# Kernel optimization log

Hardware: AMD Instinct MI355X
Metric: run time of the kernel (lower is better)

The kernel has to match this reference:

```python
import jax, jax.numpy as jnp
import numpy as np


def _gen_grid(h, w, stride=1):
    """Normalized spherical sampling grid, shape (3*H', 3*W', 2) with (x, y) order,
    matching gen_grid_coordinates in the torch source (vectorized)."""
    pi = np.pi
    dphi = pi / h
    dth = 2 * pi / w
    t = np.tan(dth)
    p = np.tan(dphi)
    sp = p / np.cos(dth)
    # xys[kr, kc] = (x, y) tangent-plane offsets of the 3x3 kernel taps
    xys = np.array([[[-t, sp], [0.0, p], [t, sp]],
                    [[-t, 0.0], [1.0, 1.0], [t, 0.0]],
                    [[-t, -sp], [0.0, -p], [t, -sp]]], dtype=np.float64)
    X = xys[..., 0]
    Y = xys[..., 1]
    rho = np.sqrt(X ** 2 + Y ** 2)           # [3,3], nonzero everywhere
    v = np.arctan(rho)
    rr = np.arange(0, h, stride)
    cc = np.arange(0, w, stride)
    phi = -((rr + 0.5) / h * pi - pi / 2)    # [H']
    theta = (cc + 0.5) / w * 2 * pi - pi     # [W']
    sphi = np.sin(phi)[:, None, None, None]  # [H',1,1,1]
    cphi = np.cos(phi)[:, None, None, None]
    arg = np.cos(v) * sphi + Y * np.sin(v) * cphi / rho  # [H',1,3,3]
    new_phi = np.arcsin(np.clip(arg, -1.0, 1.0))
    new_theta = theta[None, :, None, None] + np.arctan(
        X * np.sin(v) / (rho * cphi * np.cos(v) - Y * sphi * np.sin(v)))  # [H',W',3,3]
    new_r = np.broadcast_to((-new_phi + pi / 2) * h / pi - 0.5, new_theta.shape).copy()
    new_c = (new_theta + pi) * w / (2 * pi) - 0.5
    new_c = (new_c + w) % w
    # center tap samples the pixel itself
    new_r[:, :, 1, 1] = rr[:, None]
    new_c[:, :, 1, 1] = cc[None, :]
    gx = new_c * 2 / w - 1
    gy = new_r * 2 / h - 1
    grid = np.stack([gx, gy], axis=-1)                     # [H',W',3,3,2]
    Hp, Wp = len(rr), len(cc)
    grid = grid.transpose(0, 2, 1, 3, 4).reshape(Hp * 3, Wp * 3, 2)
    return grid.astype(np.float32)


def _grid_sample_bilinear_zeros(x, grid):
    """torch grid_sample(mode='bilinear', padding_mode='zeros', align_corners=False).
    x: [N,C,H,W]; grid: [Hg,Wg,2] (shared over batch). Returns [N,C,Hg,Wg]."""
    N, C, H, W = x.shape
    ix = ((grid[..., 0] + 1) * W - 1) * 0.5
    iy = ((grid[..., 1] + 1) * H - 1) * 0.5
    x0 = jnp.floor(ix)
    y0 = jnp.floor(iy)
    x1 = x0 + 1
    y1 = y0 + 1
    wx1 = ix - x0
    wx0 = 1.0 - wx1
    wy1 = iy - y0
    wy0 = 1.0 - wy1

    def gather(yy, xx):
        valid = ((xx >= 0) & (xx <= W - 1) & (yy >= 0) & (yy <= H - 1)).astype(x.dtype)
        xi = jnp.clip(xx, 0, W - 1).astype(jnp.int32)
        yi = jnp.clip(yy, 0, H - 1).astype(jnp.int32)
        return x[:, :, yi, xi], valid  # [N,C,Hg,Wg], [Hg,Wg]

    v00, m00 = gather(y0, x0)
    v01, m01 = gather(y0, x1)
    v10, m10 = gather(y1, x0)
    v11, m11 = gather(y1, x1)
    return (v00 * (wy0 * wx0 * m00) + v01 * (wy0 * wx1 * m01)
            + v10 * (wy1 * wx0 * m10) + v11 * (wy1 * wx1 * m11))


def setup_inputs() -> dict:
    key = jax.random.key(0)
    k1, k2, k3 = jax.random.split(key, 3)
    N, Cin, H, W = 4, 64, 128, 256
    Cout = 128
    x = jax.random.normal(k1, (N, Cin, H, W), dtype=jnp.float32)
    fan_in = Cin * 9
    bound = 1.0 / np.sqrt(fan_in)
    weight = jax.random.uniform(k2, (Cout, Cin, 3, 3), dtype=jnp.float32,
                                minval=-bound, maxval=bound)
    bias = jnp.zeros((Cout,), dtype=jnp.float32)
    return {"x": x, "weight": weight, "bias": bias}


def reference(x, weight, bias):
    H, W = int(x.shape[2]), int(x.shape[3])
    grid = jnp.asarray(_gen_grid(H, W, 1))              # [3H, 3W, 2]
    s = _grid_sample_bilinear_zeros(x, grid)            # [N, Cin, 3H, 3W]
    y = jax.lax.conv_general_dilated(
        s, weight, window_strides=(3, 3), padding='VALID',
        dimension_numbers=('NCHW', 'OIHW', 'NCHW'))     # [N, Cout, H, W]
    return y + bias[None, :, None, None]
```

## Files before the change

kernel.cpp:

```cpp
#include <hip/hip_runtime.h>
#include <math.h>

typedef __attribute__((ext_vector_type(8))) _Float16 half8;
typedef __attribute__((ext_vector_type(4))) _Float16 half4;
typedef __attribute__((ext_vector_type(2))) _Float16 half2;
typedef __attribute__((ext_vector_type(4))) float floatx4;
typedef __attribute__((ext_vector_type(4))) unsigned int uintx4;

#define NB    4
#define CIN   64
#define COUT  128
#define IMH   128
#define IMW   256
#define KTOT  576
#define NPIX  (IMH * IMW)
#define PXT   128
#define NDPB  (PXT * 9)
#define ROWS  4
#define KCH   96
#define DSTR  520
#define XT_OFF 262144
#define XT_BYTES ((size_t)NB * 8 * IMH * IMW * 16)

__device__ __forceinline__ unsigned pkrtz2(float a, float b) {
  unsigned r;
  asm("v_cvt_pkrtz_f16_f32 %0, %1, %2" : "=v"(r) : "v"(a), "v"(b));
  return r;
}
__device__ __forceinline__ half4 bcl(unsigned u) {
  half2 h; __builtin_memcpy(&h, &u, 4);
  return __builtin_shufflevector(h, h, 0, 0, 0, 0);
}
__device__ __forceinline__ half4 bch(unsigned u) {
  half2 h; __builtin_memcpy(&h, &u, 4);
  return __builtin_shufflevector(h, h, 1, 1, 1, 1);
}
__device__ __forceinline__ half8 bcl8(unsigned u) {
  half2 h; __builtin_memcpy(&h, &u, 4);
  return __builtin_shufflevector(h, h, 0, 0, 0, 0, 0, 0, 0, 0);
}
__device__ __forceinline__ half8 bch8(unsigned u) {
  half2 h; __builtin_memcpy(&h, &u, 4);
  return __builtin_shufflevector(h, h, 1, 1, 1, 1, 1, 1, 1, 1);
}
__device__ __forceinline__ void gload_lds16(const void* g, void* l) {
  __builtin_amdgcn_global_load_lds(
      (const __attribute__((address_space(1))) unsigned int*)g,
      (__attribute__((address_space(3))) unsigned int*)l, 16, 0, 0);
}

__global__ __launch_bounds__(256) void prep_w_kernel(const float* __restrict__ w,
                                                     unsigned short* __restrict__ wbf) {
  int idx = blockIdx.x * 256 + threadIdx.x;
  if (idx >= COUT * 8 * KCH) return;
  int co = idx / (8 * KCH);
  int K2 = idx - co * (8 * KCH);
  int cb = K2 / KCH, kk = K2 - cb * KCH;
  unsigned short v = 0;
  if (kk < 72) {
    int t = kk >> 3, chl = kk & 7;
    int ci = cb * 8 + chl;
    _Float16 h = (_Float16)w[co * KTOT + ci * 9 + t];
    __builtin_memcpy(&v, &h, 2);
  }
  wbf[(K2 >> 3) * (COUT * 8) + co * 8 + (K2 & 7)] = v;
}

__global__ __launch_bounds__(256) void prep_x_kernel(const float* __restrict__ x,
                                                     unsigned short* __restrict__ xt) {
  int idx = blockIdx.x * 256 + threadIdx.x;
  int c   = idx & 255;
  int rr  = (idx >> 8) & 127;
  int ncb = idx >> 15;
  int n = ncb >> 3, cb = ncb & 7;
  const float* src = x + (size_t)(n * CIN + cb * 8) * NPIX + rr * IMW + c;
  unsigned o4[4];
  #pragma unroll
  for (int j = 0; j < 4; j++)
    o4[j] = pkrtz2(src[(size_t)(2 * j) * NPIX], src[(size_t)(2 * j + 1) * NPIX]);
  *(uintx4*)(xt + (size_t)idx * 8) = *(uintx4*)o4;
}

__global__ __launch_bounds__(512, 4) void sphconv_fast(
    const unsigned short* __restrict__ xt, const unsigned short* __restrict__ wbf,
    const float* __restrict__ bias, float* __restrict__ out) {
  __shared__ __align__(16) unsigned int stg[2][ROWS * IMW * 4];
  __shared__ __align__(16) unsigned int descL[12 * DSTR];
  __shared__ double tapA[9];
  __shared__ float  tapWy[9][2];
  __shared__ int    tapRo[9][2];

  const int tid  = threadIdx.x;
  const int lane = tid & 63;
  const int wv   = tid >> 6;
  const int lin = blockIdx.x + 2 * blockIdx.y;
  const int sw  = (lin & 7) * 32 + (lin >> 3);
  const int ct  = sw >> 7;
  const int r   = sw & 127;
  const int n   = blockIdx.z;
  const int c0  = ct * PXT;
  const int co_base = (wv & 1) * 64;
  const int px_base = (wv >> 1) * 32;
  const int rlo  = min(max(r - 2, 0), IMH - ROWS);
  const int q    = lane >> 4;
  const int p    = lane & 15;

  {
    const char* gs = (const char*)xt
        + ((size_t)((n * 8 + 0) * IMH + rlo) * IMW) * 16 + wv * 1024 + lane * 16;
    char* lb = (char*)&stg[0][0] + wv * 1024;
    gload_lds16(gs, lb);
    gload_lds16(gs + 8192, lb + 8192);
  }

  {
    int myk = -1;
    if (lane == 0) myk = wv;
    if (wv == 0 && lane == 32) myk = 8;
    if (myk >= 0) {
      const double pi = 3.14159265358979323846;
      double dphi = pi / IMH;
      double dth  = 2.0 * pi / IMW;
      double t  = tan(dth);
      double pp = tan(dphi);
      double sp_ = pp / cos(dth);
      double phi  = -(((double)r + 0.5) / IMH * pi - pi * 0.5);
      double sphi = sin(phi), cphi = cos(phi);
      int i = myk / 3, j = myk % 3;
      double atv, new_r;
      if (myk == 4) {
        atv = 0.0; new_r = (double)r;
      } else {
        double X = (j == 0) ? -t : ((j == 2) ? t : 0.0);
        double Y = 0.0;
        if (i == 0)      Y = (j == 1) ?  pp :  sp_;
        else if (i == 2) Y = (j == 1) ? -pp : -sp_;
        double rho = sqrt(X * X + Y * Y);
        double v   = atan(rho);
        double sv = sin(v), cv = cos(v);
        double arg = cv * sphi + Y * sv * cphi / rho;
        arg = fmin(1.0, fmax(-1.0, arg));
        double new_phi = asin(arg);
        double denom = rho * cphi * cv - Y * sphi * sv;
        atv = atan(X * sv / denom);
        new_r = (-new_phi + pi * 0.5) * IMH / pi - 0.5;
      }
      float gy = (float)(new_r * 2.0 / IMH - 1.0);
      float iy = ((gy + 1.0f) * (float)IMH - 1.0f) * 0.5f;
      float fy = floorf(iy); int y0 = (int)fy;
      float wy1 = iy - fy, wy0 = 1.0f - wy1;
      int y1 = y0 + 1;
      bool vy0 = (y0 >= 0) & (y0 <= IMH - 1);
      bool vy1 = (y1 >= 0) & (y1 <= IMH - 1);
      int y0c = min(max(y0, 0), IMH - 1), y1c = min(max(y1, 0), IMH - 1);
      int rt = min(max(y0c - rlo, 0), ROWS - 1);
      int rb = min(max(y1c - rlo, 0), ROWS - 1);
      tapA[myk] = atv;
      tapWy[myk][0] = vy0 ? wy0 : 0.0f;
      tapWy[myk][1] = vy1 ? wy1 : 0.0f;
      tapRo[myk][0] = rt * (IMW * 4);
      tapRo[myk][1] = rb * (IMW * 4);
    }
  }
  __syncthreads();

  {
    const double pi = 3.14159265358979323846;
    #pragma unroll
    for (int dd = 0; dd < 3; dd++) {
      if (dd < 2 || tid < NDPB - 1024) {
        int d  = tid + dd * 512;
        int px = d & (PXT - 1), k = d >> 7;
        int c  = c0 + px;
        double nc;
        if (k == 4) {
          nc = (double)c;
        } else {
          double theta = ((double)c + 0.5) / IMW * (2.0 * pi) - pi;
          double new_theta = theta + tapA[k];
          nc = (new_theta + pi) * IMW / (2.0 * pi) - 0.5;
          nc = fmod(nc + (double)IMW, (double)IMW);
        }
        float gx = (float)(nc * 2.0 / IMW - 1.0);
        float ix = ((gx + 1.0f) * (float)IMW - 1.0f) * 0.5f;
        float fx = floorf(ix); int x0 = (int)fx;
        float wx1 = ix - fx, wx0 = 1.0f - wx1;
        int x1 = x0 + 1;
        int x0c = max(x0, 0);
        float w_lo = (x0 >= 0) ? wx0 : wx1;
        float w_hi = (x0 >= 0) ? ((x1 <= IMW - 1) ? wx1 : 0.0f) : 0.0f;
        float wy0m = tapWy[k][0], wy1m = tapWy[k][1];
        int dc = (x1 <= IMW - 1) ? 4 : 0;
        int offt = tapRo[k][0] + x0c * 4;
        int offb = tapRo[k][1] + x0c * 4;
        uintx4 rec;
        rec.x = (unsigned)(offt | (offb << 16));
        rec.y = pkrtz2(wy0m * w_lo, wy0m * w_hi);
        rec.z = pkrtz2(wy1m * w_lo, wy1m * w_hi);
        rec.w = (unsigned)dc;
        *(uintx4*)&descL[k * DSTR + px * 4] = rec;
      }
    }
  }
  if (tid < 3 * PXT) {
    uintx4 zr = {0u, 0u, 0u, 0u};
    *(uintx4*)&descL[(9 + (tid >> 7)) * DSTR + (tid & (PXT - 1)) * 4] = zr;
  }

  floatx4 acc[4][2];
  #pragma unroll
  for (int mt = 0; mt < 4; mt++)
    #pragma unroll
    for (int nt = 0; nt < 2; nt++)
      acc[mt][nt] = (floatx4){0.f, 0.f, 0.f, 0.f};

  __syncthreads();

  #pragma unroll 1
  for (int cb = 0; cb < 8; cb++) {
    if (cb < 7) {
      const char* gs = (const char*)xt
          + ((size_t)((n * 8 + cb + 1) * IMH + rlo) * IMW) * 16 + wv * 1024 + lane * 16;
      char* lb = (char*)&stg[(cb + 1) & 1][0] + wv * 1024;
      gload_lds16(gs, lb);
      gload_lds16(gs + 8192, lb + 8192);
    }
    const unsigned int* sb = &stg[cb & 1][0];
    #pragma unroll
    for (int nt = 0; nt < 2; nt++) {
      const int pxl = px_base + nt * 16 + p;
      #pragma unroll
      for (int ks = 0; ks < 3; ks++) {
        uintx4 rec = *(const uintx4*)&descL[(ks * 4 + q) * DSTR + pxl * 4];
        unsigned op = rec.x;
        int dc = (int)rec.w;
        const unsigned int* pt = sb + (op & 0xFFFFu);
        const unsigned int* pb = sb + (op >> 16);
        half8 t0 = *(const half8*)pt;
        half8 t1 = *(const half8*)(pt + dc);
        half8 b0 = *(const half8*)pb;
        half8 b1 = *(const half8*)(pb + dc);
        half8 W0 = bcl8(rec.y), W1 = bch8(rec.y);
        half8 W2 = bcl8(rec.z), W3 = bch8(rec.z);
        half8 b = t0 * W0 + t1 * W1 + b0 * W2 + b1 * W3;
        const unsigned short* arow =
            wbf + (size_t)((cb * 12 + ks * 4 + q) * COUT + co_base + p) * 8;
        __builtin_amdgcn_s_setprio(1);
        #pragma unroll
        for (int mt = 0; mt < 4; mt++) {
          half8 a = *(const half8*)(arow + mt * 16 * 8);
          acc[mt][nt] = __builtin_amdgcn_mfma_f32_16x16x32_f16(a, b, acc[mt][nt], 0, 0, 0);
        }
        __builtin_amdgcn_s_setprio(0);
      }
    }
    __syncthreads();
  }

  #pragma unroll
  for (int mt = 0; mt < 4; mt++)
    #pragma unroll
    for (int nt = 0; nt < 2; nt++)
      #pragma unroll
      for (int rg = 0; rg < 4; rg++) {
        const int co = co_base + mt * 16 + q * 4 + rg;
        const int cc = c0 + px_base + nt * 16 + p;
        out[(((size_t)n * COUT + co) * IMH + r) * IMW + cc] = acc[mt][nt][rg] + bias[co];
      }
}

#define F_CSTW  6
#define F_NCOL  257
#define F_RSTW  (F_NCOL * F_CSTW)
__global__ __launch_bounds__(512, 4) void sphconv_fb(
    const float* __restrict__ x, const unsigned short* __restrict__ wbf,
    const float* __restrict__ bias, float* __restrict__ out) {
  __shared__ __align__(16) unsigned int stg[2][ROWS * F_RSTW];
  __shared__ __align__(16) unsigned int descL[12 * PXT * 4];
  __shared__ double tapA[9];
  __shared__ float  tapWy[9][2];
  __shared__ int    tapRo[9][2];

  const int tid  = threadIdx.x;
  const int lane = tid & 63;
  const int wv   = tid >> 6;
  const int lin = blockIdx.x + 2 * blockIdx.y;
  const int sw  = (lin & 7) * 32 + (lin >> 3);
  const int ct  = sw >> 7;
  const int r   = sw & 127;
  const int n   = blockIdx.z;
  const int c0  = ct * PXT;
  const int co_base = (wv & 1) * 64;
  const int px_base = (wv >> 1) * 32;
  const int rlo  = min(max(r - 2, 0), IMH - ROWS);
  const int q    = lane >> 4;
  const int p    = lane & 15;
  const int sp  = tid & 3;
  const int scg = (tid >> 2) & 63;
  const int srr = tid >> 8;

  const float* xn = x + (size_t)n * CIN * NPIX;

  floatx4 nx[4];
  #pragma unroll
  for (int c = 0; c < 2; c++)
    #pragma unroll
    for (int rw = 0; rw < 2; rw++)
      nx[c * 2 + rw] = *(const floatx4*)(xn + (size_t)(sp * 2 + c) * NPIX
                                         + (size_t)(rlo + srr * 2 + rw) * IMW + scg * 4);

  {
    int myk = -1;
    if (lane == 0) myk = wv;
    if (wv == 0 && lane == 32) myk = 8;
    if (myk >= 0) {
      const double pi = 3.14159265358979323846;
      double dphi = pi / IMH;
      double dth  = 2.0 * pi / IMW;
      double t  = tan(dth);
      double pp = tan(dphi);
      double sp_ = pp / cos(dth);
      double phi  = -(((double)r + 0.5) / IMH * pi - pi * 0.5);
      double sphi = sin(phi), cphi = cos(phi);
      int i = myk / 3, j = myk % 3;
      double atv, new_r;
      if (myk == 4) {
        atv = 0.0; new_r = (double)r;
      } else {
        double X = (j == 0) ? -t : ((j == 2) ? t : 0.0);
        double Y = 0.0;
        if (i == 0)      Y = (j == 1) ?  pp :  sp_;
        else if (i == 2) Y = (j == 1) ? -pp : -sp_;
        double rho = sqrt(X * X + Y * Y);
        double v   = atan(rho);
        double sv = sin(v), cv = cos(v);
        double arg = cv * sphi + Y * sv * cphi / rho;
        arg = fmin(1.0, fmax(-1.0, arg));
        double new_phi = asin(arg);
        double denom = rho * cphi * cv - Y * sphi * sv;
        atv = atan(X * sv / denom);
        new_r = (-new_phi + pi * 0.5) * IMH / pi - 0.5;
      }
      float gy = (float)(new_r * 2.0 / IMH - 1.0);
      float iy = ((gy + 1.0f) * (float)IMH - 1.0f) * 0.5f;
      float fy = floorf(iy); int y0 = (int)fy;
      float wy1 = iy - fy, wy0 = 1.0f - wy1;
      int y1 = y0 + 1;
      bool vy0 = (y0 >= 0) & (y0 <= IMH - 1);
      bool vy1 = (y1 >= 0) & (y1 <= IMH - 1);
      int y0c = min(max(y0, 0), IMH - 1), y1c = min(max(y1, 0), IMH - 1);
      int rt = min(max(y0c - rlo, 0), ROWS - 1);
      int rb = min(max(y1c - rlo, 0), ROWS - 1);
      tapA[myk] = atv;
      tapWy[myk][0] = vy0 ? wy0 : 0.0f;
      tapWy[myk][1] = vy1 ? wy1 : 0.0f;
      tapRo[myk][0] = rt * F_RSTW;
      tapRo[myk][1] = rb * F_RSTW;
    }
  }
  __syncthreads();

  {
    const double pi = 3.14159265358979323846;
    #pragma unroll
    for (int dd = 0; dd < 3; dd++) {
      if (dd < 2 || tid < NDPB - 1024) {
        int d  = tid + dd * 512;
        int px = d & (PXT - 1), k = d >> 7;
        int c  = c0 + px;
        double nc;
        if (k == 4) {
          nc = (double)c;
        } else {
          double theta = ((double)c + 0.5) / IMW * (2.0 * pi) - pi;
          double new_theta = theta + tapA[k];
          nc = (new_theta + pi) * IMW / (2.0 * pi) - 0.5;
          nc = fmod(nc + (double)IMW, (double)IMW);
        }
        float gx = (float)(nc * 2.0 / IMW - 1.0);
        float ix = ((gx + 1.0f) * (float)IMW - 1.0f) * 0.5f;
        float fx = floorf(ix); int x0 = (int)fx;
        float wx1 = ix - fx, wx0 = 1.0f - wx1;
        int x1 = x0 + 1;
        int x0c = max(x0, 0);
        float w_lo = (x0 >= 0) ? wx0 : wx1;
        float w_hi = (x0 >= 0) ? ((x1 <= IMW - 1) ? wx1 : 0.0f) : 0.0f;
        float wy0m = tapWy[k][0], wy1m = tapWy[k][1];
        int sh0 = ((x0c >> 4) & 1) * 2;
        int sh1 = (((x0c + 1) >> 4) & 1) * 2;
        int dc  = F_CSTW + sh1 - sh0;
        int offt = tapRo[k][0] + x0c * F_CSTW + sh0;
        int offb = tapRo[k][1] + x0c * F_CSTW + sh0;
        uintx4 rec;
        rec.x = (unsigned)(offt | (offb << 16));
        rec.y = pkrtz2(wy0m * w_lo, wy0m * w_hi);
        rec.z = pkrtz2(wy1m * w_lo, wy1m * w_hi);
        rec.w = (unsigned)dc;
        *(uintx4*)&descL[(k * PXT + px) * 4] = rec;
      }
    }
  }
  if (tid < 3 * PXT) {
    uintx4 zr = {0u, 0u, 0u, (unsigned)F_CSTW};
    *(uintx4*)&descL[((9 + (tid >> 7)) * PXT + (tid & (PXT - 1))) * 4] = zr;
  }

  #pragma unroll
  for (int rw = 0; rw < 2; rw++)
    #pragma unroll
    for (int i = 0; i < 4; i++) {
      int col = scg * 4 + i;
      int sh = ((col >> 4) & 1) * 2;
      stg[0][(srr * 2 + rw) * F_RSTW + col * F_CSTW + sh + sp] =
          pkrtz2(nx[rw][i], nx[2 + rw][i]);
    }
  if (tid < 32) stg[tid >> 4][((tid >> 2) & 3) * F_RSTW + 256 * F_CSTW + (tid & 3)] = 0u;

  floatx4 acc[4][2];
  #pragma unroll
  for (int mt = 0; mt < 4; mt++)
    #pragma unroll
    for (int nt = 0; nt < 2; nt++)
      acc[mt][nt] = (floatx4){0.f, 0.f, 0.f, 0.f};

  __syncthreads();

  #pragma unroll 1
  for (int cb = 0; cb < 8; cb++) {
    if (cb < 7) {
      #pragma unroll
      for (int c = 0; c < 2; c++)
        #pragma unroll
        for (int rw = 0; rw < 2; rw++)
          nx[c * 2 + rw] = *(const floatx4*)(xn + (size_t)((cb + 1) * 8 + sp * 2 + c) * NPIX
                                             + (size_t)(rlo + srr * 2 + rw) * IMW + scg * 4);
    }
    const unsigned int* sb = &stg[cb & 1][0];
    #pragma unroll
    for (int nt = 0; nt < 2; nt++) {
      const int pxl = px_base + nt * 16 + p;
      #pragma unroll
      for (int ks = 0; ks < 3; ks++) {
        uintx4 rec = *(const uintx4*)&descL[((ks * 4 + q) * PXT + pxl) * 4];
        unsigned op = rec.x;
        int dc = (int)rec.w;
        const unsigned int* pt = sb + (op & 0xFFFFu);
        const unsigned int* pb = sb + (op >> 16);
        half4 t0  = *(const half4*)(pt);
        half4 t0h = *(const half4*)(pt + 2);
        half4 t1  = *(const half4*)(pt + dc);
        half4 t1h = *(const half4*)(pt + dc + 2);
        half4 b0  = *(const half4*)(pb);
        half4 b0h = *(const half4*)(pb + 2);
        half4 b1  = *(const half4*)(pb + dc);
        half4 b1h = *(const half4*)(pb + dc + 2);
        half4 W0 = bcl(rec.y), W1 = bch(rec.y);
        half4 W2 = bcl(rec.z), W3 = bch(rec.z);
        half4 slo = t0 * W0 + t1 * W1 + b0 * W2 + b1 * W3;
        half4 shi = t0h * W0 + t1h * W1 + b0h * W2 + b1h * W3;
        half8 b = __builtin_shufflevector(slo, shi, 0, 1, 2, 3, 4, 5, 6, 7);
        const unsigned short* arow =
            wbf + (size_t)((cb * 12 + ks * 4 + q) * COUT + co_base + p) * 8;
        __builtin_amdgcn_s_setprio(1);
        #pragma unroll
        for (int mt = 0; mt < 4; mt++) {
          half8 a = *(const half8*)(arow + mt * 16 * 8);
          acc[mt][nt] = __builtin_amdgcn_mfma_f32_16x16x32_f16(a, b, acc[mt][nt], 0, 0, 0);
        }
        __builtin_amdgcn_s_setprio(0);
      }
    }
    if (cb < 7) {
      #pragma unroll
      for (int rw = 0; rw < 2; rw++)
        #pragma unroll
        for (int i = 0; i < 4; i++) {
          int col = scg * 4 + i;
          int sh = ((col >> 4) & 1) * 2;
          stg[(cb + 1) & 1][(srr * 2 + rw) * F_RSTW + col * F_CSTW + sh + sp] =
              pkrtz2(nx[rw][i], nx[2 + rw][i]);
        }
    }
    __syncthreads();
  }

  #pragma unroll
  for (int mt = 0; mt < 4; mt++)
    #pragma unroll
    for (int nt = 0; nt < 2; nt++)
      #pragma unroll
      for (int rg = 0; rg < 4; rg++) {
        const int co = co_base + mt * 16 + q * 4 + rg;
        const int cc = c0 + px_base + nt * 16 + p;
        out[(((size_t)n * COUT + co) * IMH + r) * IMW + cc] = acc[mt][nt][rg] + bias[co];
      }
}

extern "C" void kernel_launch(void* const* d_in, const int* in_sizes, int n_in,
                              void* d_out, int out_size, void* d_ws, size_t ws_size,
                              hipStream_t stream) {
  const float* x    = (const float*)d_in[0];
  const float* w    = (const float*)d_in[1];
  const float* bias = (const float*)d_in[2];
  float* out = (float*)d_out;
  unsigned short* wbf = (unsigned short*)d_ws;
  (void)in_sizes; (void)n_in; (void)out_size;

  hipLaunchKernelGGL(prep_w_kernel, dim3((COUT * 8 * KCH + 255) / 256), dim3(256), 0, stream, w, wbf);
  if (ws_size >= (size_t)XT_OFF + XT_BYTES) {
    unsigned short* xt = (unsigned short*)((char*)d_ws + XT_OFF);
    hipLaunchKernelGGL(prep_x_kernel, dim3((NB * 8 * IMH * IMW) / 256), dim3(256), 0, stream, x, xt);
    hipLaunchKernelGGL(sphconv_fast, dim3(IMW / PXT, IMH, NB), dim3(512), 0, stream,
                       xt, wbf, bias, out);
  } else {
    hipLaunchKernelGGL(sphconv_fb, dim3(IMW / PXT, IMH, NB), dim3(512), 0, stream,
                       x, wbf, bias, out);
  }
}
```

Before: 164.2 us.

## Retile waves to cover all output channels for 16 pixels, sharing interpolated B

Each wave now computes all 128 output channels for a 16-pixel slice instead of 64 channels for 32 pixels. The bilinear-interpolated B fragment is computed once and reused across eight MFMAs, eliminating the duplicate LDS gathers and interpolation work that two waves previously did for the same pixels. The cost is twice as many weight fragment loads per wave from global memory, and descriptor records are preloaded for all three ks steps.

```diff
diff --git a/kernel.cpp b/kernel.cpp
--- a/kernel.cpp
+++ b/kernel.cpp
@@ -99,11 +99,10 @@
   const int r   = sw & 127;
   const int n   = blockIdx.z;
   const int c0  = ct * PXT;
-  const int co_base = (wv & 1) * 64;
-  const int px_base = (wv >> 1) * 32;
   const int rlo  = min(max(r - 2, 0), IMH - ROWS);
   const int q    = lane >> 4;
   const int p    = lane & 15;
+  const int pxl  = wv * 16 + p;
 
   {
     const char* gs = (const char*)xt
@@ -207,12 +206,10 @@
     *(uintx4*)&descL[(9 + (tid >> 7)) * DSTR + (tid & (PXT - 1)) * 4] = zr;
   }
 
-  floatx4 acc[4][2];
-  #pragma unroll
-  for (int mt = 0; mt < 4; mt++)
-    #pragma unroll
-    for (int nt = 0; nt < 2; nt++)
-      acc[mt][nt] = (floatx4){0.f, 0.f, 0.f, 0.f};
+  floatx4 acc[8];
+  #pragma unroll
+  for (int mt = 0; mt < 8; mt++)
+    acc[mt] = (floatx4){0.f, 0.f, 0.f, 0.f};
 
   __syncthreads();
 
@@ -226,47 +223,44 @@
       gload_lds16(gs + 8192, lb + 8192);
     }
     const unsigned int* sb = &stg[cb & 1][0];
-    #pragma unroll
-    for (int nt = 0; nt < 2; nt++) {
-      const int pxl = px_base + nt * 16 + p;
+    uintx4 rec[3];
+    #pragma unroll
+    for (int ks = 0; ks < 3; ks++)
+      rec[ks] = *(const uintx4*)&descL[(ks * 4 + q) * DSTR + pxl * 4];
+    #pragma unroll
+    for (int ks = 0; ks < 3; ks++) {
+      unsigned op = rec[ks].x;
+      int dc = (int)rec[ks].w;
+      const unsigned int* pt = sb + (op & 0xFFFFu);
+      const unsigned int* pb = sb + (op >> 16);
+      half8 t0 = *(const half8*)pt;
+      half8 t1 = *(const half8*)(pt + dc);
+      half8 b0 = *(const half8*)pb;
+      half8 b1 = *(const half8*)(pb + dc);
+      half8 W0 = bcl8(rec[ks].y), W1 = bch8(rec[ks].y);
+      half8 W2 = bcl8(rec[ks].z), W3 = bch8(rec[ks].z);
+      half8 b = t0 * W0 + t1 * W1 + b0 * W2 + b1 * W3;
+      const unsigned short* arow =
+          wbf + (size_t)((cb * 12 + ks * 4 + q) * COUT + p) * 8;
+      __builtin_amdgcn_s_setprio(1);
       #pragma unroll
-      for (int ks = 0; ks < 3; ks++) {
-        uintx4 rec = *(const uintx4*)&descL[(ks * 4 + q) * DSTR + pxl * 4];
-        unsigned op = rec.x;
-        int dc = (int)rec.w;
-        const unsigned int* pt = sb + (op & 0xFFFFu);
-        const unsigned int* pb = sb + (op >> 16);
-        half8 t0 = *(const half8*)pt;
-        half8 t1 = *(const half8*)(pt + dc);
-        half8 b0 = *(const half8*)pb;
-        half8 b1 = *(const half8*)(pb + dc);
-        half8 W0 = bcl8(rec.y), W1 = bch8(rec.y);
-        half8 W2 = bcl8(rec.z), W3 = bch8(rec.z);
-        half8 b = t0 * W0 + t1 * W1 + b0 * W2 + b1 * W3;
-        const unsigned short* arow =
-            wbf + (size_t)((cb * 12 + ks * 4 + q) * COUT + co_base + p) * 8;
-        __builtin_amdgcn_s_setprio(1);
-        #pragma unroll
-        for (int mt = 0; mt < 4; mt++) {
-          half8 a = *(const half8*)(arow + mt * 16 * 8);
-          acc[mt][nt] = __builtin_amdgcn_mfma_f32_16x16x32_f16(a, b, acc[mt][nt], 0, 0, 0);
-        }
-        __builtin_amdgcn_s_setprio(0);
-      }
+      for (int mt = 0; mt < 8; mt++) {
+        half8 a = *(const half8*)(arow + mt * 16 * 8);
+        acc[mt] = __builtin_amdgcn_mfma_f32_16x16x32_f16(a, b, acc[mt], 0, 0, 0);
+      }
+      __builtin_amdgcn_s_setprio(0);
     }
     __syncthreads();
   }
 
   #pragma unroll
-  for (int mt = 0; mt < 4; mt++)
-    #pragma unroll
-    for (int nt = 0; nt < 2; nt++)
-      #pragma unroll
-      for (int rg = 0; rg < 4; rg++) {
-        const int co = co_base + mt * 16 + q * 4 + rg;
-        const int cc = c0 + px_base + nt * 16 + p;
-        out[(((size_t)n * COUT + co) * IMH + r) * IMW + cc] = acc[mt][nt][rg] + bias[co];
-      }
+  for (int mt = 0; mt < 8; mt++)
+    #pragma unroll
+    for (int rg = 0; rg < 4; rg++) {
+      const int co = mt * 16 + q * 4 + rg;
+      const int cc = c0 + pxl;
+      out[(((size_t)n * COUT + co) * IMH + r) * IMW + cc] = acc[mt][rg] + bias[co];
+    }
 }
 
 #define F_CSTW  6
```

Measured after the change: 165.3 us. Within noise of the previous version (+0.7%).
